# Kernel tuning notes

Measured on AMD Instinct MI355X. Metric: run time of the kernel, lower is better.

Reference implementation:

```python
import jax, jax.numpy as jnp
import numpy as np

NUM_HEADS = 16
MASK_VALUE = -10000.0


def setup_inputs() -> dict:
    key = jax.random.key(0)
    ks = jax.random.split(key, 5)
    B, S, D = 2, 2048, 1024
    std = 0.02
    return {
        "hidden_states": jax.random.normal(ks[0], (B, S, D), dtype=jnp.float32),
        "wq": jax.random.normal(ks[1], (D, D), dtype=jnp.float32) * std,
        "bq": jnp.zeros((D,), dtype=jnp.float32),
        "wk": jax.random.normal(ks[2], (D, D), dtype=jnp.float32) * std,
        "bk": jnp.zeros((D,), dtype=jnp.float32),
        "wv": jax.random.normal(ks[3], (D, D), dtype=jnp.float32) * std,
        "bv": jnp.zeros((D,), dtype=jnp.float32),
        "wc": jax.random.normal(ks[4], (D, D), dtype=jnp.float32) * std,
        "bc": jnp.zeros((D,), dtype=jnp.float32),
    }


def reference(hidden_states, wq, bq, wk, bk, wv, bv, wc, bc):
    B, S, D = hidden_states.shape
    H = NUM_HEADS
    hd = D // H

    def split_heads(x):  # [B,S,D] -> [B,H,S,hd]
        return x.reshape(B, S, H, hd).transpose(0, 2, 1, 3)

    q = split_heads(hidden_states @ wq + bq)
    k = split_heads(hidden_states @ wk + bk)
    v = split_heads(hidden_states @ wv + bv)

    # eager QK^T with scale_attn_weights (divide by sqrt(head_dim))
    attn_weights = jnp.einsum("bhqd,bhkd->bhqk", q, k) / jnp.sqrt(
        jnp.asarray(hd, dtype=q.dtype))

    # causal mask (attention_mask is None, not cross-attention)
    causal = jnp.tril(jnp.ones((S, S), dtype=bool))[None, None]
    attn_weights = jnp.where(causal, attn_weights,
                             jnp.asarray(MASK_VALUE, dtype=attn_weights.dtype))

    attn_weights = jax.nn.softmax(attn_weights, axis=-1)
    # attn_dropout p=0.0 (eval) -> identity; no head_mask

    attn_output = jnp.einsum("bhqk,bhkd->bhqd", attn_weights, v)
    attn_output = attn_output.transpose(0, 2, 1, 3).reshape(B, S, D)
    attn_output = attn_output @ wc + bc  # c_proj; resid_dropout p=0 -> identity
    return attn_output, attn_weights, k, v
```

## Files before the change

### kernel.cpp

```cpp
#include <hip/hip_runtime.h>


typedef __attribute__((ext_vector_type(8))) short bf8_t;
typedef __attribute__((ext_vector_type(4))) float f4_t;

#define MFMA(a, b, c) __builtin_amdgcn_mfma_f32_16x16x32_bf16(a, b, c, 0, 0, 0)

static __device__ __forceinline__ unsigned short f2bf(float f) {
    union { float f; unsigned u; } x; x.f = f;
    unsigned u = x.u;
    return (unsigned short)((u + 0x7fffu + ((u >> 16) & 1u)) >> 16);
}

static __device__ __forceinline__ void stage16(const unsigned short* g, unsigned short* lbase) {
    __builtin_amdgcn_global_load_lds(
        (const __attribute__((address_space(1))) unsigned int*)g,
        (__attribute__((address_space(3))) unsigned int*)lbase, 16, 0, 0);
}

#define NE 4194304ULL
#define AW 134217728ULL


__global__ void cast_hidden(const float* __restrict__ src, unsigned short* __restrict__ dst) {
    int i = (blockIdx.x * 256 + threadIdx.x) * 4;
    float4 h = *(const float4*)(src + i);
    ushort4 o;
    o.x = f2bf(h.x); o.y = f2bf(h.y); o.z = f2bf(h.z); o.w = f2bf(h.w);
    *(ushort4*)(dst + i) = o;
}

__global__ void transpose_w(const float* __restrict__ wq, const float* __restrict__ wk,
                            const float* __restrict__ wv, const float* __restrict__ wc,
                            unsigned short* __restrict__ wqkvT, unsigned short* __restrict__ wcT) {
    __shared__ float tile[32][33];
    int z = blockIdx.z;
    const float* W = z == 0 ? wq : z == 1 ? wk : z == 2 ? wv : wc;
    unsigned short* dst = (z < 3) ? (wqkvT + (size_t)z * 1024 * 1024) : wcT;
    int x0 = blockIdx.x * 32, y0 = blockIdx.y * 32;
    int tx = threadIdx.x, ty = threadIdx.y;
#pragma unroll
    for (int i = 0; i < 4; ++i)
        tile[ty + i * 8][tx] = W[(size_t)(y0 + ty + i * 8) * 1024 + x0 + tx];
    __syncthreads();
#pragma unroll
    for (int i = 0; i < 4; ++i)
        dst[(size_t)(x0 + ty + i * 8) * 1024 + y0 + tx] = f2bf(tile[tx][ty + i * 8]);
}


#define GEMM_CORE(A_, B_, KDIM)                                                             \
    const int m0 = blockIdx.y * 128, n0 = blockIdx.x * 128;                                 \
    const int tid = threadIdx.x, w = tid >> 6, lane = tid & 63, ln = lane & 15,             \
              quad = lane >> 4;                                                             \
    const int wm = (w & 1) * 64, wn = (w >> 1) * 64;                                        \
    f4_t acc[4][4] = {};                                                                    \
    for (int kb = 0; kb < (KDIM); kb += 64) {                                               \
        __syncthreads();                                                                    \
        _Pragma("unroll")                                                                   \
        for (int p = 0; p < 4; ++p) {                                                       \
            int t = (w * 4 + p) * 64 + lane;                                                \
            int r = t >> 3, c = (t & 7) ^ (r & 7);                                          \
            stage16(&(A_)[(size_t)(m0 + r) * (KDIM) + kb + c * 8], &As[(w * 4 + p) * 512]); \
            stage16(&(B_)[(size_t)(n0 + r) * (KDIM) + kb + c * 8], &Bs[(w * 4 + p) * 512]); \
        }                                                                                   \
        __syncthreads();                                                                    \
        bf8_t af[2][4], bfm[2][4];                                                          \
        _Pragma("unroll")                                                                   \
        for (int h = 0; h < 2; ++h) {                                                       \
            _Pragma("unroll")                                                               \
            for (int i = 0; i < 4; ++i) {                                                   \
                int c = (h * 4 + quad) ^ (ln & 7);                                          \
                af[h][i] = *(const bf8_t*)&As[(wm + i * 16 + ln) * 64 + c * 8];             \
                bfm[h][i] = *(const bf8_t*)&Bs[(wn + i * 16 + ln) * 64 + c * 8];            \
            }                                                                               \
        }                                                                                   \
        _Pragma("unroll")                                                                   \
        for (int h = 0; h < 2; ++h)                                                         \
            _Pragma("unroll")                                                               \
            for (int i = 0; i < 4; ++i)                                                     \
                _Pragma("unroll")                                                           \
                for (int j = 0; j < 4; ++j)                                                 \
                    acc[i][j] = MFMA(af[h][i], bfm[h][j], acc[i][j]);                       \
    }

__global__ __launch_bounds__(256) void gemm_qkv(
    const unsigned short* __restrict__ A, const unsigned short* __restrict__ BT,
    const float* __restrict__ bq, const float* __restrict__ bk, const float* __restrict__ bv,
    unsigned short* __restrict__ q_bf, unsigned short* __restrict__ k_bf,
    unsigned short* __restrict__ vT_bf, float* __restrict__ out_k, float* __restrict__ out_v)
{
    __shared__ __align__(16) unsigned short As[128 * 64];
    __shared__ __align__(16) unsigned short Bs[128 * 64];
    GEMM_CORE(A, BT, 1024)
#pragma unroll
    for (int j = 0; j < 4; ++j) {
        int coln = n0 + wn + j * 16 + ln;
        int which = coln >> 10, d = coln & 1023, h = d >> 6, e = d & 63;
        float bias = which == 0 ? bq[d] : (which == 1 ? bk[d] : bv[d]);
#pragma unroll
        for (int i = 0; i < 4; ++i) {
#pragma unroll
            for (int v = 0; v < 4; ++v) {
                int row = m0 + wm + i * 16 + quad * 4 + v;
                int b = row >> 11, s = row & 2047;
                float val = acc[i][j][v] + bias;
                size_t hidx = (((size_t)(b * 16 + h)) * 2048 + s) * 64 + e;
                if (which == 0) {
                    q_bf[hidx] = f2bf(val * 0.125f);
                } else if (which == 1) {
                    k_bf[hidx] = f2bf(val);
                    __builtin_nontemporal_store(val, &out_k[hidx]);
                } else {
                    vT_bf[((size_t)(b * 16 + h) * 64 + e) * 2048 + s] = f2bf(val);
                    __builtin_nontemporal_store(val, &out_v[hidx]);
                }
            }
        }
    }
}

__global__ __launch_bounds__(256) void gemm_cproj(
    const unsigned short* __restrict__ A, const unsigned short* __restrict__ BT,
    const float* __restrict__ bc, float* __restrict__ out)
{
    __shared__ __align__(16) unsigned short As[128 * 64];
    __shared__ __align__(16) unsigned short Bs[128 * 64];
    GEMM_CORE(A, BT, 1024)
#pragma unroll
    for (int j = 0; j < 4; ++j) {
        int coln = n0 + wn + j * 16 + ln;
        float bias = bc[coln];
#pragma unroll
        for (int i = 0; i < 4; ++i) {
#pragma unroll
            for (int v = 0; v < 4; ++v) {
                int row = m0 + wm + i * 16 + quad * 4 + v;
                __builtin_nontemporal_store(acc[i][j][v] + bias, &out[(size_t)row * 1024 + coln]);
            }
        }
    }
}

__global__ __launch_bounds__(256) void attn_fused(
    const unsigned short* __restrict__ q_bf,
    const unsigned short* __restrict__ k_bf,
    const unsigned short* __restrict__ vT_bf,
    float* __restrict__ attn_w,
    unsigned short* __restrict__ attnpre)
{
    __shared__ __align__(16) float Pf32[4][16 * 36];
    const int bh = blockIdx.x;
    const int q0 = (31 - blockIdx.y) * 64;
    const int tid = threadIdx.x, w = tid >> 6, lane = tid & 63, ln = lane & 15, quad = lane >> 4;
    const int g0 = q0 + w * 16;
    const int rmax = g0 + 15;
    const unsigned short* qb = q_bf + ((size_t)bh * 2048 + g0) * 64;
    bf8_t aA0 = *(const bf8_t*)&qb[(size_t)ln * 64 + quad * 8];
    bf8_t aA1 = *(const bf8_t*)&qb[(size_t)ln * 64 + 32 + quad * 8];
    const unsigned short* kb_base = k_bf + (size_t)bh * 2048 * 64;
    const f4_t zf = {0.f, 0.f, 0.f, 0.f};

    f4_t lv = {0.f, 0.f, 0.f, 0.f};
    const int nkt = (rmax >> 4) + 1;
    for (int kt = 0; kt < nkt; ++kt) {
        int col = kt * 16 + ln;
        const unsigned short* kp = kb_base + (size_t)col * 64 + quad * 8;
        bf8_t b0 = *(const bf8_t*)kp;
        bf8_t b1 = *(const bf8_t*)(kp + 32);
        f4_t sc = MFMA(aA0, b0, zf); sc = MFMA(aA1, b1, sc);
#pragma unroll
        for (int v = 0; v < 4; ++v) {
            if (col <= g0 + quad * 4 + v) lv[v] += __expf(sc[v]);
        }
    }
#pragma unroll
    for (int m = 1; m < 16; m <<= 1) {
#pragma unroll
        for (int v = 0; v < 4; ++v) lv[v] += __shfl_xor(lv[v], m);
    }
    f4_t linv;
#pragma unroll
    for (int v = 0; v < 4; ++v) linv[v] = 1.f / lv[v];

    f4_t o[4] = {};
    float* awp = attn_w + (size_t)bh * 2048 * 2048;
    const unsigned short* vt_base = vT_bf + (size_t)bh * 64 * 2048;
    float* pw = &Pf32[w][0];
    const int nact = (rmax >> 5) + 1;
    for (int kc = 0; kc < nact; ++kc) {
        int col0c = kc * 32;
        bf8_t kf[4], vb[4];
#pragma unroll
        for (int sub = 0; sub < 2; ++sub) {
            const unsigned short* kp = kb_base + (size_t)(col0c + sub * 16 + ln) * 64 + quad * 8;
            kf[sub * 2] = *(const bf8_t*)kp;
            kf[sub * 2 + 1] = *(const bf8_t*)(kp + 32);
        }
#pragma unroll
        for (int j = 0; j < 4; ++j)
            vb[j] = *(const bf8_t*)(vt_base + (size_t)(j * 16 + ln) * 2048 + col0c + quad * 8);
#pragma unroll
        for (int sub = 0; sub < 2; ++sub) {
            f4_t sc = MFMA(aA0, kf[sub * 2], zf);
            sc = MFMA(aA1, kf[sub * 2 + 1], sc);
            int col = col0c + sub * 16 + ln;
#pragma unroll
            for (int v = 0; v < 4; ++v) {
                int row = g0 + quad * 4 + v;
                float p = (col <= row) ? __expf(sc[v]) * linv[v] : 0.f;
                pw[(quad * 4 + v) * 36 + sub * 16 + ln] = p;
            }
        }
#pragma unroll
        for (int half = 0; half < 2; ++half) {
            int r = half * 8 + (lane >> 3), cq = lane & 7;
            f4_t val = *(const f4_t*)&pw[r * 36 + cq * 4];
            __builtin_nontemporal_store(val, (f4_t*)&awp[(size_t)(g0 + r) * 2048 + col0c + cq * 4]);
        }
        f4_t pa = *(const f4_t*)&pw[ln * 36 + quad * 8];
        f4_t pb = *(const f4_t*)&pw[ln * 36 + quad * 8 + 4];
        bf8_t pf;
        pf[0] = (short)f2bf(pa[0]); pf[1] = (short)f2bf(pa[1]);
        pf[2] = (short)f2bf(pa[2]); pf[3] = (short)f2bf(pa[3]);
        pf[4] = (short)f2bf(pb[0]); pf[5] = (short)f2bf(pb[1]);
        pf[6] = (short)f2bf(pb[2]); pf[7] = (short)f2bf(pb[3]);
#pragma unroll
        for (int j = 0; j < 4; ++j) o[j] = MFMA(pf, vb[j], o[j]);
    }
    {
        const f4_t z4 = {0.f, 0.f, 0.f, 0.f};
        int r = (lane >> 3), cq = lane & 7;
        float* aw0 = awp + (size_t)(g0 + r) * 2048 + cq * 4;
        for (int kc = nact; kc < 64; ++kc) {
            int col0c = kc * 32;
#pragma unroll
            for (int half = 0; half < 2; ++half)
                __builtin_nontemporal_store(z4, (f4_t*)(aw0 + (size_t)half * 8 * 2048 + col0c));
        }
    }
    int b = bh >> 4, h = bh & 15;
#pragma unroll
    for (int j = 0; j < 4; ++j) {
#pragma unroll
        for (int v = 0; v < 4; ++v) {
            int e = h * 64 + j * 16 + ln;
            attnpre[(size_t)(b * 2048 + g0 + quad * 4 + v) * 1024 + e] = f2bf(o[j][v]);
        }
    }
}

extern "C" void kernel_launch(void* const* d_in, const int* in_sizes, int n_in,
                              void* d_out, int out_size, void* d_ws, size_t ws_size,
                              hipStream_t stream)
{
    const float* hs = (const float*)d_in[0];
    const float* wq = (const float*)d_in[1];
    const float* bq = (const float*)d_in[2];
    const float* wk = (const float*)d_in[3];
    const float* bk = (const float*)d_in[4];
    const float* wv = (const float*)d_in[5];
    const float* bv = (const float*)d_in[6];
    const float* wc = (const float*)d_in[7];
    const float* bc = (const float*)d_in[8];

    float* out      = (float*)d_out;
    float* out_aw   = out + NE;
    float* out_k    = out_aw + AW;
    float* out_v    = out_k + NE;

    char* ws = (char*)d_ws;
    unsigned short* hid_bf  = (unsigned short*)(ws);
    unsigned short* wqkvT   = (unsigned short*)(ws + 8388608);
    unsigned short* wcT     = (unsigned short*)(ws + 14680064);
    unsigned short* q_bf    = (unsigned short*)(ws + 16777216);
    unsigned short* k_bf    = (unsigned short*)(ws + 25165824);
    unsigned short* vT_bf   = (unsigned short*)(ws + 33554432);
    unsigned short* attnpre = (unsigned short*)(ws + 41943040);

    cast_hidden<<<4096, 256, 0, stream>>>(hs, hid_bf);
    transpose_w<<<dim3(32, 32, 4), dim3(32, 8), 0, stream>>>(wq, wk, wv, wc, wqkvT, wcT);
    gemm_qkv<<<dim3(24, 32), 256, 0, stream>>>(hid_bf, wqkvT, bq, bk, bv,
                                               q_bf, k_bf, vT_bf, out_k, out_v);
    attn_fused<<<dim3(32, 32), 256, 0, stream>>>(q_bf, k_bf, vT_bf, out_aw, attnpre);
    gemm_cproj<<<dim3(8, 32), 256, 0, stream>>>(attnpre, wcT, bc, out);
}
```

Measured before the change: 808.7 us.

## Single-pass attention with unnormalized fp16 probabilities buffered in LDS

The attention kernel now computes exp scores once rather than twice. It keeps unnormalized probabilities for a full 16-row strip in a large fp16 LDS buffer and normalizes afterwards when writing attn_weights and the PV output. Work is split across four warps by column stride, with partial sums combined through LDS atomics. V is stored in fp16 so the PV product can use the f16 MFMA. This removes the separate row-sum pass over K, at the cost of about 66 KB of LDS per block, which lowers occupancy. It also adds LDS atomics and rounds the probabilities to fp16 before they are written out as fp32 weights.

```diff
diff --git a/kernel.cpp b/kernel.cpp
--- a/kernel.cpp
+++ b/kernel.cpp
@@ -3,8 +3,11 @@
 
 typedef __attribute__((ext_vector_type(8))) short bf8_t;
 typedef __attribute__((ext_vector_type(4))) float f4_t;
-
-#define MFMA(a, b, c) __builtin_amdgcn_mfma_f32_16x16x32_bf16(a, b, c, 0, 0, 0)
+typedef __attribute__((ext_vector_type(8))) _Float16 h8_t;
+typedef __attribute__((ext_vector_type(4))) _Float16 h4_t;
+
+#define MFMA(a, b, c)  __builtin_amdgcn_mfma_f32_16x16x32_bf16(a, b, c, 0, 0, 0)
+#define MFMAH(a, b, c) __builtin_amdgcn_mfma_f32_16x16x32_f16(a, b, c, 0, 0, 0)
 
 static __device__ __forceinline__ unsigned short f2bf(float f) {
     union { float f; unsigned u; } x; x.f = f;
@@ -88,7 +91,7 @@
     const unsigned short* __restrict__ A, const unsigned short* __restrict__ BT,
     const float* __restrict__ bq, const float* __restrict__ bk, const float* __restrict__ bv,
     unsigned short* __restrict__ q_bf, unsigned short* __restrict__ k_bf,
-    unsigned short* __restrict__ vT_bf, float* __restrict__ out_k, float* __restrict__ out_v)
+    _Float16* __restrict__ vT_h, float* __restrict__ out_k, float* __restrict__ out_v)
 {
     __shared__ __align__(16) unsigned short As[128 * 64];
     __shared__ __align__(16) unsigned short Bs[128 * 64];
@@ -112,7 +115,7 @@
                     k_bf[hidx] = f2bf(val);
                     __builtin_nontemporal_store(val, &out_k[hidx]);
                 } else {
-                    vT_bf[((size_t)(b * 16 + h) * 64 + e) * 2048 + s] = f2bf(val);
+                    vT_h[((size_t)(b * 16 + h) * 64 + e) * 2048 + s] = (_Float16)val;
                     __builtin_nontemporal_store(val, &out_v[hidx]);
                 }
             }
@@ -142,111 +145,111 @@
     }
 }
 
+#define PB 2064
+
 __global__ __launch_bounds__(256) void attn_fused(
     const unsigned short* __restrict__ q_bf,
     const unsigned short* __restrict__ k_bf,
-    const unsigned short* __restrict__ vT_bf,
+    const _Float16* __restrict__ vT_h,
     float* __restrict__ attn_w,
     unsigned short* __restrict__ attnpre)
 {
-    __shared__ __align__(16) float Pf32[4][16 * 36];
+    __shared__ _Float16 Pbuf[16 * PB];
+    __shared__ float oatom[16][68];
+    __shared__ float lred[16];
     const int bh = blockIdx.x;
-    const int q0 = (31 - blockIdx.y) * 64;
+    const int g0 = (127 - (int)blockIdx.y) * 16;
     const int tid = threadIdx.x, w = tid >> 6, lane = tid & 63, ln = lane & 15, quad = lane >> 4;
-    const int g0 = q0 + w * 16;
-    const int rmax = g0 + 15;
+
+    if (tid < 16) lred[tid] = 0.f;
+#pragma unroll
+    for (int i = 0; i < 5; ++i) {
+        int s = tid + i * 256;
+        if (s < 16 * 68) ((float*)oatom)[s] = 0.f;
+    }
+    __syncthreads();
+
     const unsigned short* qb = q_bf + ((size_t)bh * 2048 + g0) * 64;
     bf8_t aA0 = *(const bf8_t*)&qb[(size_t)ln * 64 + quad * 8];
     bf8_t aA1 = *(const bf8_t*)&qb[(size_t)ln * 64 + 32 + quad * 8];
     const unsigned short* kb_base = k_bf + (size_t)bh * 2048 * 64;
+    const _Float16* vt_base = vT_h + (size_t)bh * 64 * 2048;
     const f4_t zf = {0.f, 0.f, 0.f, 0.f};
+    const int cend = ((g0 + 16 + 31) >> 5) << 5;
 
     f4_t lv = {0.f, 0.f, 0.f, 0.f};
-    const int nkt = (rmax >> 4) + 1;
-    for (int kt = 0; kt < nkt; ++kt) {
-        int col = kt * 16 + ln;
-        const unsigned short* kp = kb_base + (size_t)col * 64 + quad * 8;
-        bf8_t b0 = *(const bf8_t*)kp;
-        bf8_t b1 = *(const bf8_t*)(kp + 32);
-        f4_t sc = MFMA(aA0, b0, zf); sc = MFMA(aA1, b1, sc);
-#pragma unroll
-        for (int v = 0; v < 4; ++v) {
-            if (col <= g0 + quad * 4 + v) lv[v] += __expf(sc[v]);
-        }
-    }
-#pragma unroll
-    for (int m = 1; m < 16; m <<= 1) {
-#pragma unroll
-        for (int v = 0; v < 4; ++v) lv[v] += __shfl_xor(lv[v], m);
-    }
-    f4_t linv;
-#pragma unroll
-    for (int v = 0; v < 4; ++v) linv[v] = 1.f / lv[v];
-
     f4_t o[4] = {};
-    float* awp = attn_w + (size_t)bh * 2048 * 2048;
-    const unsigned short* vt_base = vT_bf + (size_t)bh * 64 * 2048;
-    float* pw = &Pf32[w][0];
-    const int nact = (rmax >> 5) + 1;
-    for (int kc = 0; kc < nact; ++kc) {
-        int col0c = kc * 32;
-        bf8_t kf[4], vb[4];
+    for (int c = w * 32; c < cend; c += 128) {
+        bf8_t kf[4];
+        h8_t vb[4];
 #pragma unroll
         for (int sub = 0; sub < 2; ++sub) {
-            const unsigned short* kp = kb_base + (size_t)(col0c + sub * 16 + ln) * 64 + quad * 8;
+            const unsigned short* kp = kb_base + (size_t)(c + sub * 16 + ln) * 64 + quad * 8;
             kf[sub * 2] = *(const bf8_t*)kp;
             kf[sub * 2 + 1] = *(const bf8_t*)(kp + 32);
         }
 #pragma unroll
         for (int j = 0; j < 4; ++j)
-            vb[j] = *(const bf8_t*)(vt_base + (size_t)(j * 16 + ln) * 2048 + col0c + quad * 8);
+            vb[j] = *(const h8_t*)(vt_base + (size_t)(j * 16 + ln) * 2048 + c + quad * 8);
 #pragma unroll
         for (int sub = 0; sub < 2; ++sub) {
             f4_t sc = MFMA(aA0, kf[sub * 2], zf);
             sc = MFMA(aA1, kf[sub * 2 + 1], sc);
-            int col = col0c + sub * 16 + ln;
+            int col = c + sub * 16 + ln;
 #pragma unroll
             for (int v = 0; v < 4; ++v) {
                 int row = g0 + quad * 4 + v;
-                float p = (col <= row) ? __expf(sc[v]) * linv[v] : 0.f;
-                pw[(quad * 4 + v) * 36 + sub * 16 + ln] = p;
+                float p = (col <= row) ? __expf(sc[v]) : 0.f;
+                lv[v] += p;
+                Pbuf[(quad * 4 + v) * PB + col] = (_Float16)p;
             }
         }
-#pragma unroll
-        for (int half = 0; half < 2; ++half) {
-            int r = half * 8 + (lane >> 3), cq = lane & 7;
-            f4_t val = *(const f4_t*)&pw[r * 36 + cq * 4];
-            __builtin_nontemporal_store(val, (f4_t*)&awp[(size_t)(g0 + r) * 2048 + col0c + cq * 4]);
-        }
-        f4_t pa = *(const f4_t*)&pw[ln * 36 + quad * 8];
-        f4_t pb = *(const f4_t*)&pw[ln * 36 + quad * 8 + 4];
-        bf8_t pf;
-        pf[0] = (short)f2bf(pa[0]); pf[1] = (short)f2bf(pa[1]);
-        pf[2] = (short)f2bf(pa[2]); pf[3] = (short)f2bf(pa[3]);
-        pf[4] = (short)f2bf(pb[0]); pf[5] = (short)f2bf(pb[1]);
-        pf[6] = (short)f2bf(pb[2]); pf[7] = (short)f2bf(pb[3]);
-#pragma unroll
-        for (int j = 0; j < 4; ++j) o[j] = MFMA(pf, vb[j], o[j]);
-    }
-    {
-        const f4_t z4 = {0.f, 0.f, 0.f, 0.f};
-        int r = (lane >> 3), cq = lane & 7;
-        float* aw0 = awp + (size_t)(g0 + r) * 2048 + cq * 4;
-        for (int kc = nact; kc < 64; ++kc) {
-            int col0c = kc * 32;
-#pragma unroll
-            for (int half = 0; half < 2; ++half)
-                __builtin_nontemporal_store(z4, (f4_t*)(aw0 + (size_t)half * 8 * 2048 + col0c));
-        }
-    }
+        h8_t pf = *(const h8_t*)&Pbuf[ln * PB + c + quad * 8];
+#pragma unroll
+        for (int j = 0; j < 4; ++j) o[j] = MFMAH(pf, vb[j], o[j]);
+    }
+
+#pragma unroll
+    for (int m = 1; m < 16; m <<= 1) {
+#pragma unroll
+        for (int v = 0; v < 4; ++v) lv[v] += __shfl_xor(lv[v], m);
+    }
+    if (ln == 0) {
+#pragma unroll
+        for (int v = 0; v < 4; ++v) atomicAdd(&lred[quad * 4 + v], lv[v]);
+    }
+#pragma unroll
+    for (int j = 0; j < 4; ++j)
+#pragma unroll
+        for (int v = 0; v < 4; ++v)
+            atomicAdd(&oatom[quad * 4 + v][j * 16 + ln], o[j][v]);
+    __syncthreads();
+
+    float* awp = attn_w + ((size_t)bh * 2048 + g0) * 2048;
+#pragma unroll
+    for (int rr = 0; rr < 4; ++rr) {
+        int row = w * 4 + rr;
+        float linv_r = 1.f / lred[row];
+        float* dst = awp + (size_t)row * 2048;
+#pragma unroll
+        for (int i = 0; i < 8; ++i) {
+            int col = i * 256 + lane * 4;
+            h4_t ph = *(const h4_t*)&Pbuf[row * PB + col];
+            f4_t val;
+#pragma unroll
+            for (int j = 0; j < 4; ++j)
+                val[j] = (col + j < cend) ? (float)ph[j] * linv_r : 0.f;
+            __builtin_nontemporal_store(val, (f4_t*)(dst + col));
+        }
+    }
+
     int b = bh >> 4, h = bh & 15;
 #pragma unroll
-    for (int j = 0; j < 4; ++j) {
-#pragma unroll
-        for (int v = 0; v < 4; ++v) {
-            int e = h * 64 + j * 16 + ln;
-            attnpre[(size_t)(b * 2048 + g0 + quad * 4 + v) * 1024 + e] = f2bf(o[j][v]);
-        }
+    for (int rr = 0; rr < 4; ++rr) {
+        int row = w * 4 + rr;
+        float linv_r = 1.f / lred[row];
+        attnpre[(size_t)(b * 2048 + g0 + row) * 1024 + h * 64 + lane] =
+            f2bf(oatom[row][lane] * linv_r);
     }
 }
 
@@ -275,13 +278,13 @@
     unsigned short* wcT     = (unsigned short*)(ws + 14680064);
     unsigned short* q_bf    = (unsigned short*)(ws + 16777216);
     unsigned short* k_bf    = (unsigned short*)(ws + 25165824);
-    unsigned short* vT_bf   = (unsigned short*)(ws + 33554432);
+    _Float16*       vT_h    = (_Float16*)(ws + 33554432);
     unsigned short* attnpre = (unsigned short*)(ws + 41943040);
 
     cast_hidden<<<4096, 256, 0, stream>>>(hs, hid_bf);
     transpose_w<<<dim3(32, 32, 4), dim3(32, 8), 0, stream>>>(wq, wk, wv, wc, wqkvT, wcT);
     gemm_qkv<<<dim3(24, 32), 256, 0, stream>>>(hid_bf, wqkvT, bq, bk, bv,
-                                               q_bf, k_bf, vT_bf, out_k, out_v);
-    attn_fused<<<dim3(32, 32), 256, 0, stream>>>(q_bf, k_bf, vT_bf, out_aw, attnpre);
+                                               q_bf, k_bf, vT_h, out_k, out_v);
+    attn_fused<<<dim3(32, 128), 256, 0, stream>>>(q_bf, k_bf, vT_h, out_aw, attnpre);
     gemm_cproj<<<dim3(8, 32), 256, 0, stream>>>(attnpre, wcT, bc, out);
 }
```

New measurement: 814.0 us. About the same (+0.6%).
